# Kernel tuning notes

Measured on AMD Instinct MI355X. Metric: run time of the kernel, lower is better.

The kernel has to match this reference:

```python
import jax, jax.numpy as jnp
import numpy as np

TAU = 2.0      # LIF membrane time constant
VTH = 1.0      # firing threshold
ALPHA = 4.0    # sigmoid surrogate sharpness (spikingjelly default)
EPS = 1e-5     # BatchNorm eps


@jax.custom_vjp
def spike(x):
    # Heaviside forward, sigmoid surrogate backward
    return (x >= 0.0).astype(x.dtype)

def _spike_fwd(x):
    return (x >= 0.0).astype(x.dtype), x

def _spike_bwd(x, g):
    s = jax.nn.sigmoid(ALPHA * x)
    return (g * ALPHA * s * (1.0 - s),)

spike.defvjp(_spike_fwd, _spike_bwd)


def setup_inputs() -> dict:
    key = jax.random.key(0)
    k1, k2 = jax.random.split(key)
    T, B, C_in, C_out, M = 8, 16, 256, 256, 1024
    x = jax.random.normal(k1, (T, B, C_in, M), dtype=jnp.float32)
    W = jax.random.normal(k2, (C_out, C_in), dtype=jnp.float32) * 0.05  # 1x1 conv weight
    gamma = jnp.ones((C_out,), dtype=jnp.float32)
    beta = jnp.zeros((C_out,), dtype=jnp.float32)
    return {"x": x, "W": W, "gamma": gamma, "beta": beta}


def reference(x, W, gamma, beta):
    # 1x1 Conv1d over flattened (T*B) batch == channel contraction
    y = jnp.einsum('oc,tbcm->tbom', W, x)  # [T,B,C_out,M]
    # BatchNorm1d (training forward): per-channel stats over (T*B, M)
    mean = y.mean(axis=(0, 1, 3), keepdims=True)
    var = y.var(axis=(0, 1, 3), keepdims=True)
    y = (y - mean) * jax.lax.rsqrt(var + EPS)
    y = y * gamma[None, None, :, None] + beta[None, None, :, None]

    # Multi-step LIF: v <- v + (x - v)/tau; fire; hard reset to 0 (detached)
    def step(v, xt):
        v = v + (xt - v) / TAU
        s = spike(v - VTH)
        v = v * (1.0 - jax.lax.stop_gradient(s))
        return v, s

    v0 = jnp.zeros_like(y[0])
    _, spikes = jax.lax.scan(step, v0, y)
    return spikes  # [T,B,C_out,M]
```

## Files before the change

### kernel.cpp

```cpp
#include <hip/hip_runtime.h>

#define TT 8
#define BB 16
#define CC 256
#define MM 1024
#define NY 33554432


__global__ __launch_bounds__(256) void einsum_store_mean(
    const float* __restrict__ x, const float* __restrict__ W,
    float* __restrict__ y, float* __restrict__ part)
{
    __shared__ float wt[CC][16];
    __shared__ float yrow[4][1056];
    __shared__ float scratch[4][64];
    const int tid = threadIdx.x;
    const int lin = blockIdx.x;
    const int xcd = lin & 7;
    const int j   = lin >> 3;
    const int og  = j & 15;
    const int tb  = xcd * 16 + (j >> 4);
    const int m0  = tid * 4;

#pragma unroll
    for (int i = 0; i < 16; ++i)
        wt[tid][i] = W[(size_t)(og * 16 + i) * CC + tid];
    __syncthreads();

    const float* xs = x + (size_t)tb * (CC * MM) + m0;

    float a[16][4];
#pragma unroll
    for (int i = 0; i < 16; ++i)
#pragma unroll
        for (int q = 0; q < 4; ++q) a[i][q] = 0.0f;

    float4 xb[4];
#pragma unroll
    for (int q = 0; q < 4; ++q)
        xb[q] = *(const float4*)(xs + (size_t)q * MM);

    for (int cb = 0; cb < CC; cb += 4) {
        float4 xn[4];
        const bool more = (cb + 4 < CC);
        if (more) {
#pragma unroll
            for (int q = 0; q < 4; ++q)
                xn[q] = *(const float4*)(xs + (size_t)(cb + 4 + q) * MM);
        }
#pragma unroll
        for (int q = 0; q < 4; ++q) {
            const int c = cb + q;
            const float4 w0 = *(const float4*)&wt[c][0];
            const float4 w1 = *(const float4*)&wt[c][4];
            const float4 w2 = *(const float4*)&wt[c][8];
            const float4 w3 = *(const float4*)&wt[c][12];
            const float wv[16] = {w0.x, w0.y, w0.z, w0.w,
                                  w1.x, w1.y, w1.z, w1.w,
                                  w2.x, w2.y, w2.z, w2.w,
                                  w3.x, w3.y, w3.z, w3.w};
#pragma unroll
            for (int i = 0; i < 16; ++i) {
                a[i][0] = __fadd_rn(a[i][0], __fmul_rn(wv[i], xb[q].x));
                a[i][1] = __fadd_rn(a[i][1], __fmul_rn(wv[i], xb[q].y));
                a[i][2] = __fadd_rn(a[i][2], __fmul_rn(wv[i], xb[q].z));
                a[i][3] = __fadd_rn(a[i][3], __fmul_rn(wv[i], xb[q].w));
            }
        }
        if (more) {
#pragma unroll
            for (int q = 0; q < 4; ++q) xb[q] = xn[q];
        }
    }

#pragma unroll
    for (int i = 0; i < 16; ++i) {
        const int o = og * 16 + i;
        *(float4*)(y + ((size_t)tb * CC + o) * MM + m0) =
            make_float4(a[i][0], a[i][1], a[i][2], a[i][3]);
    }

    const int g    = tid >> 6;
    const int lane = tid & 63;
    const int blk  = m0 >> 7;
    const int off  = m0 & 127;
#pragma unroll
    for (int r = 0; r < 4; ++r) {
        __syncthreads();
#pragma unroll
        for (int g2 = 0; g2 < 4; ++g2) {
            const int i = r * 4 + g2;
            *(float4*)&yrow[g2][blk * 132 + off] =
                make_float4(a[i][0], a[i][1], a[i][2], a[i][3]);
        }
        __syncthreads();
        {
            const int b2 = lane >> 3;
            const int k  = lane & 7;
            const float* p = &yrow[g][b2 * 132 + k];
            float rr = p[0];
#pragma unroll
            for (int i2 = 1; i2 < 16; ++i2) rr = __fadd_rn(rr, p[8 * i2]);
            scratch[g][lane] = rr;
        }
        __syncthreads();
        if (lane == 0) {
            float Bv[8];
#pragma unroll
            for (int b2 = 0; b2 < 8; ++b2) {
                const float* rp = &scratch[g][b2 * 8];
                const float s01 = __fadd_rn(rp[0], rp[1]);
                const float s23 = __fadd_rn(rp[2], rp[3]);
                const float s45 = __fadd_rn(rp[4], rp[5]);
                const float s67 = __fadd_rn(rp[6], rp[7]);
                Bv[b2] = __fadd_rn(__fadd_rn(s01, s23), __fadd_rn(s45, s67));
            }
            const float c0 = __fadd_rn(Bv[0], Bv[1]);
            const float c1 = __fadd_rn(Bv[2], Bv[3]);
            const float c2 = __fadd_rn(Bv[4], Bv[5]);
            const float c3 = __fadd_rn(Bv[6], Bv[7]);
            part[(size_t)tb * 256 + og * 16 + r * 4 + g] =
                __fadd_rn(__fadd_rn(c0, c1), __fadd_rn(c2, c3));
        }
    }
}

__global__ void reduce_mean(const float* __restrict__ part,
                            float* __restrict__ mv)
{
    const int o = threadIdx.x;
    float S = 0.0f;
    for (int tb = 0; tb < 128; ++tb)
        S = __fadd_rn(S, part[(size_t)tb * 256 + o]);
    mv[o] = S * (1.0f / 131072.0f);
}

__global__ __launch_bounds__(256) void var_partial_y(
    const float* __restrict__ y, const float* __restrict__ mv,
    float* __restrict__ part)
{
    __shared__ float yrow[4][1024];
    __shared__ float scratch[4][64];
    const int tid  = threadIdx.x;
    const int g    = tid >> 6;
    const int lane = tid & 63;
    const size_t row = (size_t)blockIdx.x * 4 + g;
    const float* yr = y + row * MM;
    const float mean = mv[row & 255];

#pragma unroll
    for (int q = 0; q < 4; ++q) {
        const float4 yv = *(const float4*)(yr + q * 256 + lane * 4);
        const float d0 = __fsub_rn(yv.x, mean);
        const float d1 = __fsub_rn(yv.y, mean);
        const float d2 = __fsub_rn(yv.z, mean);
        const float d3 = __fsub_rn(yv.w, mean);
        *(float4*)&yrow[g][q * 256 + lane * 4] =
            make_float4(__fmul_rn(d0, d0), __fmul_rn(d1, d1),
                        __fmul_rn(d2, d2), __fmul_rn(d3, d3));
    }
    __syncthreads();

    {
        const int blk = lane >> 3;
        const int k   = lane & 7;
        const float* p = &yrow[g][blk * 128 + k];
        float r = p[0];
#pragma unroll
        for (int i = 1; i < 16; ++i) r = __fadd_rn(r, p[8 * i]);
        scratch[g][lane] = r;
    }
    __syncthreads();

    if (lane == 0) {
        float B[8];
#pragma unroll
        for (int b2 = 0; b2 < 8; ++b2) {
            const float* r = &scratch[g][b2 * 8];
            const float s01 = __fadd_rn(r[0], r[1]);
            const float s23 = __fadd_rn(r[2], r[3]);
            const float s45 = __fadd_rn(r[4], r[5]);
            const float s67 = __fadd_rn(r[6], r[7]);
            B[b2] = __fadd_rn(__fadd_rn(s01, s23), __fadd_rn(s45, s67));
        }
        const float c0 = __fadd_rn(B[0], B[1]);
        const float c1 = __fadd_rn(B[2], B[3]);
        const float c2 = __fadd_rn(B[4], B[5]);
        const float c3 = __fadd_rn(B[6], B[7]);
        part[row] = __fadd_rn(__fadd_rn(c0, c1), __fadd_rn(c2, c3));
    }
}

__global__ __launch_bounds__(256) void lif_from_y(
    const float* __restrict__ y, const float* __restrict__ mv,
    const float* __restrict__ part,
    const float* __restrict__ gamma, const float* __restrict__ beta,
    float* __restrict__ out)
{
    const int tid = threadIdx.x;
    const int o = blockIdx.x;
    const int b = blockIdx.y;
    const int m0 = tid * 4;

    const float mean = mv[o];

    float S = 0.0f;
    for (int tb = 0; tb < 128; ++tb)
        S = __fadd_rn(S, part[(size_t)tb * 256 + o]);
    const float var = S * (1.0f / 131072.0f);
    const float vp  = __fadd_rn(var, 1e-5f);
    const float rs  = __fdiv_rn(1.0f, __fsqrt_rn(vp));

    const float g    = gamma[o];
    const float be   = beta[o];

    float v0 = 0.0f, v1 = 0.0f, v2 = 0.0f, v3 = 0.0f;

    for (int t = 0; t < TT; ++t) {
        const size_t off = ((size_t)(t * BB + b) * CC + o) * MM + m0;
        const float4 yv = *(const float4*)(y + off);

        const float n0 = __fadd_rn(__fmul_rn(__fmul_rn(__fsub_rn(yv.x, mean), rs), g), be);
        const float n1 = __fadd_rn(__fmul_rn(__fmul_rn(__fsub_rn(yv.y, mean), rs), g), be);
        const float n2 = __fadd_rn(__fmul_rn(__fmul_rn(__fsub_rn(yv.z, mean), rs), g), be);
        const float n3 = __fadd_rn(__fmul_rn(__fmul_rn(__fsub_rn(yv.w, mean), rs), g), be);

        v0 = __fadd_rn(v0, __fmul_rn(__fsub_rn(n0, v0), 0.5f));
        v1 = __fadd_rn(v1, __fmul_rn(__fsub_rn(n1, v1), 0.5f));
        v2 = __fadd_rn(v2, __fmul_rn(__fsub_rn(n2, v2), 0.5f));
        v3 = __fadd_rn(v3, __fmul_rn(__fsub_rn(n3, v3), 0.5f));

        const bool s0 = (v0 >= 1.0f);
        const bool s1 = (v1 >= 1.0f);
        const bool s2 = (v2 >= 1.0f);
        const bool s3 = (v3 >= 1.0f);
        if (s0) v0 = 0.0f;
        if (s1) v1 = 0.0f;
        if (s2) v2 = 0.0f;
        if (s3) v3 = 0.0f;

        *(float4*)(out + off) = make_float4(s0 ? 1.0f : 0.0f, s1 ? 1.0f : 0.0f,
                                            s2 ? 1.0f : 0.0f, s3 ? 1.0f : 0.0f);
    }
}

__global__ void reduce_var(const float* __restrict__ part,
                           float* __restrict__ mv)
{
    const int o = threadIdx.x;
    float S = 0.0f;
    for (int tb = 0; tb < 128; ++tb)
        S = __fadd_rn(S, part[(size_t)tb * 256 + o]);
    const float var = S * (1.0f / 131072.0f);
    const float vp  = __fadd_rn(var, 1e-5f);
    mv[256 + o] = __fdiv_rn(1.0f, __fsqrt_rn(vp));
}

__device__ __forceinline__ void e1_row4(
    const float* __restrict__ x, const float* __restrict__ W,
    int t, int b, int o, int m0,
    float& y0, float& y1, float& y2, float& y3)
{
    const float* xs = x + ((size_t)(t * BB + b) * CC) * MM + m0;
    const float* wr = W + (size_t)o * CC;
    y0 = 0.0f; y1 = 0.0f; y2 = 0.0f; y3 = 0.0f;
    for (int c = 0; c < CC; ++c) {
        const float wc = wr[c];
        const float4 xv = *(const float4*)(xs + (size_t)c * MM);
        y0 = __fadd_rn(y0, __fmul_rn(wc, xv.x));
        y1 = __fadd_rn(y1, __fmul_rn(wc, xv.y));
        y2 = __fadd_rn(y2, __fmul_rn(wc, xv.z));
        y3 = __fadd_rn(y3, __fmul_rn(wc, xv.w));
    }
}

__device__ __forceinline__ float np_pairwise_1024(
    const float* __restrict__ yrow, float* __restrict__ scratch, int tid)
{
    if (tid < 64) {
        const int blk = tid >> 3;
        const int k   = tid & 7;
        const float* p = yrow + blk * 128 + k;
        float r = p[0];
#pragma unroll
        for (int i = 1; i < 16; ++i) r = __fadd_rn(r, p[8 * i]);
        scratch[tid] = r;
    }
    __syncthreads();
    if (tid == 0) {
        float B[8];
#pragma unroll
        for (int blk = 0; blk < 8; ++blk) {
            const float* r = scratch + blk * 8;
            const float s01 = __fadd_rn(r[0], r[1]);
            const float s23 = __fadd_rn(r[2], r[3]);
            const float s45 = __fadd_rn(r[4], r[5]);
            const float s67 = __fadd_rn(r[6], r[7]);
            B[blk] = __fadd_rn(__fadd_rn(s01, s23), __fadd_rn(s45, s67));
        }
        const float c0 = __fadd_rn(B[0], B[1]);
        const float c1 = __fadd_rn(B[2], B[3]);
        const float c2 = __fadd_rn(B[4], B[5]);
        const float c3 = __fadd_rn(B[6], B[7]);
        scratch[64] = __fadd_rn(__fadd_rn(c0, c1), __fadd_rn(c2, c3));
    }
    __syncthreads();
    return scratch[64];
}

__global__ __launch_bounds__(256) void pass_mean_fb(
    const float* __restrict__ x, const float* __restrict__ W,
    float* __restrict__ part)
{
    __shared__ float yrow[1024];
    __shared__ float scratch[65];
    const int tid = threadIdx.x;
    const int o  = blockIdx.x;
    const int tb = blockIdx.y;
    const int m0 = tid * 4;
    float y0, y1, y2, y3;
    e1_row4(x, W, tb >> 4, tb & 15, o, m0, y0, y1, y2, y3);
    *(float4*)&yrow[m0] = make_float4(y0, y1, y2, y3);
    __syncthreads();
    const float P = np_pairwise_1024(yrow, scratch, tid);
    if (tid == 0) part[(size_t)tb * 256 + o] = P;
}

__global__ __launch_bounds__(256) void pass_var_fb(
    const float* __restrict__ x, const float* __restrict__ W,
    const float* __restrict__ mv, float* __restrict__ part)
{
    __shared__ float yrow[1024];
    __shared__ float scratch[65];
    const int tid = threadIdx.x;
    const int o  = blockIdx.x;
    const int tb = blockIdx.y;
    const int m0 = tid * 4;
    const float mean = mv[o];
    float y0, y1, y2, y3;
    e1_row4(x, W, tb >> 4, tb & 15, o, m0, y0, y1, y2, y3);
    const float d0 = __fsub_rn(y0, mean);
    const float d1 = __fsub_rn(y1, mean);
    const float d2 = __fsub_rn(y2, mean);
    const float d3 = __fsub_rn(y3, mean);
    *(float4*)&yrow[m0] = make_float4(__fmul_rn(d0, d0), __fmul_rn(d1, d1),
                                      __fmul_rn(d2, d2), __fmul_rn(d3, d3));
    __syncthreads();
    const float P = np_pairwise_1024(yrow, scratch, tid);
    if (tid == 0) part[(size_t)tb * 256 + o] = P;
}

__global__ __launch_bounds__(256) void pass_lif_fb(
    const float* __restrict__ x, const float* __restrict__ W,
    const float* __restrict__ mv,
    const float* __restrict__ gamma, const float* __restrict__ beta,
    float* __restrict__ out)
{
    const int tid = threadIdx.x;
    const int o = blockIdx.x;
    const int b = blockIdx.y;
    const int m0 = tid * 4;
    const float mean = mv[o];
    const float rs   = mv[256 + o];
    const float g    = gamma[o];
    const float be   = beta[o];
    float v0 = 0.0f, v1 = 0.0f, v2 = 0.0f, v3 = 0.0f;
    for (int t = 0; t < TT; ++t) {
        float y0, y1, y2, y3;
        e1_row4(x, W, t, b, o, m0, y0, y1, y2, y3);
        const float n0 = __fadd_rn(__fmul_rn(__fmul_rn(__fsub_rn(y0, mean), rs), g), be);
        const float n1 = __fadd_rn(__fmul_rn(__fmul_rn(__fsub_rn(y1, mean), rs), g), be);
        const float n2 = __fadd_rn(__fmul_rn(__fmul_rn(__fsub_rn(y2, mean), rs), g), be);
        const float n3 = __fadd_rn(__fmul_rn(__fmul_rn(__fsub_rn(y3, mean), rs), g), be);
        v0 = __fadd_rn(v0, __fmul_rn(__fsub_rn(n0, v0), 0.5f));
        v1 = __fadd_rn(v1, __fmul_rn(__fsub_rn(n1, v1), 0.5f));
        v2 = __fadd_rn(v2, __fmul_rn(__fsub_rn(n2, v2), 0.5f));
        v3 = __fadd_rn(v3, __fmul_rn(__fsub_rn(n3, v3), 0.5f));
        const bool s0 = (v0 >= 1.0f);
        const bool s1 = (v1 >= 1.0f);
        const bool s2 = (v2 >= 1.0f);
        const bool s3 = (v3 >= 1.0f);
        if (s0) v0 = 0.0f;
        if (s1) v1 = 0.0f;
        if (s2) v2 = 0.0f;
        if (s3) v3 = 0.0f;
        const size_t off = ((size_t)(t * BB + b) * CC + o) * MM + m0;
        *(float4*)(out + off) = make_float4(s0 ? 1.0f : 0.0f, s1 ? 1.0f : 0.0f,
                                            s2 ? 1.0f : 0.0f, s3 ? 1.0f : 0.0f);
    }
}

extern "C" void kernel_launch(void* const* d_in, const int* in_sizes, int n_in,
                              void* d_out, int out_size, void* d_ws, size_t ws_size,
                              hipStream_t stream)
{
    const float* x     = (const float*)d_in[0];
    const float* W     = (const float*)d_in[1];
    const float* gamma = (const float*)d_in[2];
    const float* beta  = (const float*)d_in[3];
    float* out = (float*)d_out;

    const size_t need = ((size_t)NY + 128 * 256 + 512) * sizeof(float);

    if (ws_size >= need) {
        float* y    = (float*)d_ws;
        float* part = y + NY;
        float* mv   = part + 128 * 256;

        einsum_store_mean<<<dim3(2048), dim3(256), 0, stream>>>(x, W, y, part);
        reduce_mean<<<dim3(1), dim3(256), 0, stream>>>(part, mv);
        var_partial_y<<<dim3(8192), dim3(256), 0, stream>>>(y, mv, part);
        lif_from_y<<<dim3(256, 16), dim3(256), 0, stream>>>(y, mv, part, gamma, beta, out);
    } else {
        float* part = (float*)d_ws;
        float* mv   = part + 128 * 256;
        pass_mean_fb<<<dim3(256, 128), dim3(256), 0, stream>>>(x, W, part);
        reduce_mean<<<dim3(1), dim3(256), 0, stream>>>(part, mv);
        pass_var_fb<<<dim3(256, 128), dim3(256), 0, stream>>>(x, W, mv, part);
        reduce_var<<<dim3(1), dim3(256), 0, stream>>>(part, mv);
        pass_lif_fb<<<dim3(256, 16), dim3(256), 0, stream>>>(x, W, mv, gamma, beta, out);
    }
}
```

Baseline: 469.5 us.

## Fold mean reduction into consumers, read weights directly, nontemporal spike stores

Drops the single-block reduce_mean launch: the variance-partial and LIF kernels now each sum the 128 mean partials themselves, and the LIF kernel reads the variance partials from a separate buffer. The GEMM kernel loads weights straight from global memory through the cache each K-step instead of staging them in LDS, which removes the LDS fill and its barrier. Spike outputs are written with nontemporal stores to limit cache pollution. The cost is redundant partial-sum reads in every block, extra global weight traffic, and a larger workspace requirement.

```diff
diff --git a/kernel.cpp b/kernel.cpp
--- a/kernel.cpp
+++ b/kernel.cpp
@@ -6,12 +6,13 @@
 #define MM 1024
 #define NY 33554432
 
+typedef float fx4 __attribute__((ext_vector_type(4)));
+
 
 __global__ __launch_bounds__(256) void einsum_store_mean(
     const float* __restrict__ x, const float* __restrict__ W,
     float* __restrict__ y, float* __restrict__ part)
 {
-    __shared__ float wt[CC][16];
     __shared__ float yrow[4][1056];
     __shared__ float scratch[4][64];
     const int tid = threadIdx.x;
@@ -22,11 +23,7 @@
     const int tb  = xcd * 16 + (j >> 4);
     const int m0  = tid * 4;
 
-#pragma unroll
-    for (int i = 0; i < 16; ++i)
-        wt[tid][i] = W[(size_t)(og * 16 + i) * CC + tid];
-    __syncthreads();
-
+    const float* __restrict__ Wp = W + (size_t)og * 16 * CC;
     const float* xs = x + (size_t)tb * (CC * MM) + m0;
 
     float a[16][4];
@@ -48,23 +45,21 @@
             for (int q = 0; q < 4; ++q)
                 xn[q] = *(const float4*)(xs + (size_t)(cb + 4 + q) * MM);
         }
+        float wqa[4][16];
+#pragma unroll
+        for (int i = 0; i < 16; ++i) {
+            const float4 wrow = *(const float4*)(Wp + (size_t)i * CC + cb);
+            wqa[0][i] = wrow.x; wqa[1][i] = wrow.y;
+            wqa[2][i] = wrow.z; wqa[3][i] = wrow.w;
+        }
 #pragma unroll
         for (int q = 0; q < 4; ++q) {
-            const int c = cb + q;
-            const float4 w0 = *(const float4*)&wt[c][0];
-            const float4 w1 = *(const float4*)&wt[c][4];
-            const float4 w2 = *(const float4*)&wt[c][8];
-            const float4 w3 = *(const float4*)&wt[c][12];
-            const float wv[16] = {w0.x, w0.y, w0.z, w0.w,
-                                  w1.x, w1.y, w1.z, w1.w,
-                                  w2.x, w2.y, w2.z, w2.w,
-                                  w3.x, w3.y, w3.z, w3.w};
 #pragma unroll
             for (int i = 0; i < 16; ++i) {
-                a[i][0] = __fadd_rn(a[i][0], __fmul_rn(wv[i], xb[q].x));
-                a[i][1] = __fadd_rn(a[i][1], __fmul_rn(wv[i], xb[q].y));
-                a[i][2] = __fadd_rn(a[i][2], __fmul_rn(wv[i], xb[q].z));
-                a[i][3] = __fadd_rn(a[i][3], __fmul_rn(wv[i], xb[q].w));
+                a[i][0] = __fadd_rn(a[i][0], __fmul_rn(wqa[q][i], xb[q].x));
+                a[i][1] = __fadd_rn(a[i][1], __fmul_rn(wqa[q][i], xb[q].y));
+                a[i][2] = __fadd_rn(a[i][2], __fmul_rn(wqa[q][i], xb[q].z));
+                a[i][3] = __fadd_rn(a[i][3], __fmul_rn(wqa[q][i], xb[q].w));
             }
         }
         if (more) {
@@ -125,6 +120,131 @@
     }
 }
 
+__global__ __launch_bounds__(256) void var_partial_im(
+    const float* __restrict__ y, const float* __restrict__ partM,
+    float* __restrict__ partV)
+{
+    __shared__ float yrow[4][1056];
+    __shared__ float scratch[4][64];
+    const int tid  = threadIdx.x;
+    const int g    = tid >> 6;
+    const int lane = tid & 63;
+    const size_t row = (size_t)blockIdx.x * 4 + g;
+    const int o = (int)(row & 255);
+    const float* yr = y + row * MM;
+
+    float S = 0.0f;
+#pragma unroll 16
+    for (int tb2 = 0; tb2 < 128; ++tb2)
+        S = __fadd_rn(S, partM[(size_t)tb2 * 256 + o]);
+    const float mean = S * (1.0f / 131072.0f);
+
+#pragma unroll
+    for (int q = 0; q < 4; ++q) {
+        const int idx = q * 256 + lane * 4;
+        const int blk = idx >> 7;
+        const int off = idx & 127;
+        const float4 yv = *(const float4*)(yr + idx);
+        const float d0 = __fsub_rn(yv.x, mean);
+        const float d1 = __fsub_rn(yv.y, mean);
+        const float d2 = __fsub_rn(yv.z, mean);
+        const float d3 = __fsub_rn(yv.w, mean);
+        *(float4*)&yrow[g][blk * 132 + off] =
+            make_float4(__fmul_rn(d0, d0), __fmul_rn(d1, d1),
+                        __fmul_rn(d2, d2), __fmul_rn(d3, d3));
+    }
+    __syncthreads();
+
+    {
+        const int b2 = lane >> 3;
+        const int k  = lane & 7;
+        const float* p = &yrow[g][b2 * 132 + k];
+        float r = p[0];
+#pragma unroll
+        for (int i = 1; i < 16; ++i) r = __fadd_rn(r, p[8 * i]);
+        scratch[g][lane] = r;
+    }
+    __syncthreads();
+
+    if (lane == 0) {
+        float B[8];
+#pragma unroll
+        for (int b2 = 0; b2 < 8; ++b2) {
+            const float* r = &scratch[g][b2 * 8];
+            const float s01 = __fadd_rn(r[0], r[1]);
+            const float s23 = __fadd_rn(r[2], r[3]);
+            const float s45 = __fadd_rn(r[4], r[5]);
+            const float s67 = __fadd_rn(r[6], r[7]);
+            B[b2] = __fadd_rn(__fadd_rn(s01, s23), __fadd_rn(s45, s67));
+        }
+        const float c0 = __fadd_rn(B[0], B[1]);
+        const float c1 = __fadd_rn(B[2], B[3]);
+        const float c2 = __fadd_rn(B[4], B[5]);
+        const float c3 = __fadd_rn(B[6], B[7]);
+        partV[row] = __fadd_rn(__fadd_rn(c0, c1), __fadd_rn(c2, c3));
+    }
+}
+
+__global__ __launch_bounds__(256) void lif_from_y_im(
+    const float* __restrict__ y, const float* __restrict__ partM,
+    const float* __restrict__ partV,
+    const float* __restrict__ gamma, const float* __restrict__ beta,
+    float* __restrict__ out)
+{
+    const int tid = threadIdx.x;
+    const int o = blockIdx.x;
+    const int b = blockIdx.y;
+    const int m0 = tid * 4;
+
+    float Sm = 0.0f;
+#pragma unroll 16
+    for (int tb = 0; tb < 128; ++tb)
+        Sm = __fadd_rn(Sm, partM[(size_t)tb * 256 + o]);
+    const float mean = Sm * (1.0f / 131072.0f);
+
+    float Sv = 0.0f;
+#pragma unroll 16
+    for (int tb = 0; tb < 128; ++tb)
+        Sv = __fadd_rn(Sv, partV[(size_t)tb * 256 + o]);
+    const float var = Sv * (1.0f / 131072.0f);
+    const float vp  = __fadd_rn(var, 1e-5f);
+    const float rs  = __fdiv_rn(1.0f, __fsqrt_rn(vp));
+
+    const float g    = gamma[o];
+    const float be   = beta[o];
+
+    float v0 = 0.0f, v1 = 0.0f, v2 = 0.0f, v3 = 0.0f;
+
+    for (int t = 0; t < TT; ++t) {
+        const size_t off = ((size_t)(t * BB + b) * CC + o) * MM + m0;
+        const float4 yv = *(const float4*)(y + off);
+
+        const float n0 = __fadd_rn(__fmul_rn(__fmul_rn(__fsub_rn(yv.x, mean), rs), g), be);
+        const float n1 = __fadd_rn(__fmul_rn(__fmul_rn(__fsub_rn(yv.y, mean), rs), g), be);
+        const float n2 = __fadd_rn(__fmul_rn(__fmul_rn(__fsub_rn(yv.z, mean), rs), g), be);
+        const float n3 = __fadd_rn(__fmul_rn(__fmul_rn(__fsub_rn(yv.w, mean), rs), g), be);
+
+        v0 = __fadd_rn(v0, __fmul_rn(__fsub_rn(n0, v0), 0.5f));
+        v1 = __fadd_rn(v1, __fmul_rn(__fsub_rn(n1, v1), 0.5f));
+        v2 = __fadd_rn(v2, __fmul_rn(__fsub_rn(n2, v2), 0.5f));
+        v3 = __fadd_rn(v3, __fmul_rn(__fsub_rn(n3, v3), 0.5f));
+
+        const bool s0 = (v0 >= 1.0f);
+        const bool s1 = (v1 >= 1.0f);
+        const bool s2 = (v2 >= 1.0f);
+        const bool s3 = (v3 >= 1.0f);
+        if (s0) v0 = 0.0f;
+        if (s1) v1 = 0.0f;
+        if (s2) v2 = 0.0f;
+        if (s3) v3 = 0.0f;
+
+        fx4 sv;
+        sv.x = s0 ? 1.0f : 0.0f; sv.y = s1 ? 1.0f : 0.0f;
+        sv.z = s2 ? 1.0f : 0.0f; sv.w = s3 ? 1.0f : 0.0f;
+        __builtin_nontemporal_store(sv, (fx4*)(out + off));
+    }
+}
+
 __global__ void reduce_mean(const float* __restrict__ part,
                             float* __restrict__ mv)
 {
@@ -205,6 +325,7 @@
     const float mean = mv[o];
 
     float S = 0.0f;
+#pragma unroll 16
     for (int tb = 0; tb < 128; ++tb)
         S = __fadd_rn(S, part[(size_t)tb * 256 + o]);
     const float var = S * (1.0f / 131072.0f);
@@ -400,9 +521,19 @@
     const float* beta  = (const float*)d_in[3];
     float* out = (float*)d_out;
 
-    const size_t need = ((size_t)NY + 128 * 256 + 512) * sizeof(float);
-
-    if (ws_size >= need) {
+    const size_t need_new = ((size_t)NY + 2 * 128 * 256) * sizeof(float);
+    const size_t need_old = ((size_t)NY + 128 * 256 + 512) * sizeof(float);
+
+    if (ws_size >= need_new) {
+        float* y     = (float*)d_ws;
+        float* partM = y + NY;
+        float* partV = partM + 128 * 256;
+
+        einsum_store_mean<<<dim3(2048), dim3(256), 0, stream>>>(x, W, y, partM);
+        var_partial_im<<<dim3(8192), dim3(256), 0, stream>>>(y, partM, partV);
+        lif_from_y_im<<<dim3(256, 16), dim3(256), 0, stream>>>(y, partM, partV,
+                                                               gamma, beta, out);
+    } else if (ws_size >= need_old) {
         float* y    = (float*)d_ws;
         float* part = y + NY;
         float* mv   = part + 128 * 256;
```

Result: faster. 445.9 us (-5.0%).
